# Kernel optimization log

Hardware: AMD Instinct MI355X
Metric: run time of the kernel (lower is better)

Reference implementation:

```python
import jax, jax.numpy as jnp
import numpy as np

B, N, F_IN, E, TOPK = 64, 1024, 64, 128, 32
NEG_SLOPE = 0.2  # GAT leaky-relu slope


def setup_inputs() -> dict:
    key = jax.random.key(0)
    ks = jax.random.split(key, 7)
    x = jax.random.normal(ks[0], (B, N, F_IN), dtype=jnp.float32)
    emb = jax.random.normal(ks[1], (N, E), dtype=jnp.float32)            # nn.Embedding table
    W_fe = jax.random.normal(ks[2], (F_IN, E), dtype=jnp.float32) / np.sqrt(F_IN).astype(np.float32)
    a_src = jax.random.normal(ks[3], (2 * E,), dtype=jnp.float32) * 0.05
    a_dst = jax.random.normal(ks[4], (2 * E,), dtype=jnp.float32) * 0.05
    lin_W = jax.random.normal(ks[5], (E, 1), dtype=jnp.float32) / np.sqrt(E).astype(np.float32)
    lin_b = jnp.zeros((1,), dtype=jnp.float32)
    return {"x": x, "emb": emb, "W_fe": W_fe, "a_src": a_src, "a_dst": a_dst,
            "lin_W": lin_W, "lin_b": lin_b}


def reference(x, emb, W_fe, a_src, a_dst, lin_W, lin_b):
    b, n, _ = x.shape
    e_dim = emb.shape[-1]
    # --- cosine-similarity topk graph construction (shared across batch) ---
    norm = jnp.linalg.norm(emb, axis=-1, keepdims=True)                  # [N,1]
    sim = (emb @ emb.T) / (norm @ norm.T)                                # [N,N]
    idx = jax.lax.top_k(sim, TOPK)[1]                                    # [N,K] int32 neighbor (target) nodes
    # --- graph attention feature extraction ---
    h = jnp.einsum('bnf,fe->bne', x, W_fe)                               # [B,N,E] projected node features
    g = jnp.concatenate([h, jnp.broadcast_to(emb, (b, n, e_dim))], -1)   # [B,N,2E] feat || embedding
    e_s = g @ a_src                                                      # [B,N] source attention term
    e_d = g @ a_dst                                                      # [B,N] target attention term
    # edges: source i repeated TOPK times -> targets idx[i]; softmax over each node's K neighbors
    scores = jax.nn.leaky_relu(e_s[:, :, None] + e_d[:, idx], NEG_SLOPE)  # [B,N,K]
    alpha = jax.nn.softmax(scores, axis=-1)                              # [B,N,K]
    h_dst = h[:, idx, :]                                                 # [B,N,K,E] gathered neighbor feats
    out = jnp.einsum('bnk,bnke->bne', alpha, h_dst)                      # aggregate messages
    out = jax.nn.relu(out)
    # --- linear readout ---
    y = out @ lin_W + lin_b                                              # [B,N,1]
    return y[..., 0]                                                     # [B,N]
```

## Files before the change

### kernel.cpp

```cpp
#include <hip/hip_runtime.h>
#include <math.h>

#define BB 64
#define NN 1024
#define F_IN 64
#define EE 128
#define TOPK 32
#define NEG_SLOPE 0.2f

typedef unsigned int uint;
typedef unsigned short ushort;
typedef unsigned long long ull;
typedef __attribute__((ext_vector_type(8))) short short8;
typedef __attribute__((ext_vector_type(4))) float f32x4;

static __device__ __forceinline__ uint f2bf(float f) {
  const uint x = __float_as_uint(f);
  return (x + 0x7fffu + ((x >> 16) & 1u)) >> 16;
}
static __device__ __forceinline__ float bf_lo(uint u) {
  return __uint_as_float(u << 16);
}
static __device__ __forceinline__ float bf_hi_raw(uint u) {
  return __uint_as_float(u);
}
static __device__ __forceinline__ uint fmono(float f) {
  uint u = __float_as_uint(f);
  return (u & 0x80000000u) ? ~u : (u | 0x80000000u);
}
static __device__ __forceinline__ ull umax64(ull a, ull b) {
  return a > b ? a : b;
}
static __device__ __forceinline__ ull umin64(ull a, ull b) {
  return a < b ? a : b;
}
static __device__ __forceinline__ ull shfl_xor64(ull v, int mask) {
  const uint lo = __shfl_xor((uint)v, mask);
  const uint hi = __shfl_xor((uint)(v >> 32), mask);
  return ((ull)hi << 32) | lo;
}

__global__ __launch_bounds__(256) void k2a_sim(
    const float* __restrict__ emb, const float* __restrict__ a_src,
    const float* __restrict__ a_dst, const float* __restrict__ W_fe,
    uint* __restrict__ keys, float* __restrict__ u_src,
    float* __restrict__ u_dst, ushort* __restrict__ wt) {
  __shared__ float ei[8][130];
  __shared__ float ej[64][130];
  const int t = threadIdx.x, wid = t >> 6, lane = t & 63;
  const int i0 = (blockIdx.x >> 2) * 8;
  const int jbase = (blockIdx.x & 3) * 256;

  if ((blockIdx.x & 3) == 0) {
    const int row = i0 + 2 * wid + (lane >> 5);
    const int ll = lane & 31;
    const float* er = emb + (size_t)row * EE;
    float us = 0.f, ud = 0.f;
#pragma unroll
    for (int c0 = 0; c0 < EE; c0 += 32) {
      const int c = c0 + ll;
      const float e = er[c];
      us += e * a_src[EE + c];
      ud += e * a_dst[EE + c];
    }
#pragma unroll
    for (int o = 1; o <= 16; o <<= 1) {
      us += __shfl_xor(us, o);
      ud += __shfl_xor(ud, o);
    }
    if (ll == 0) {
      u_src[row] = us;
      u_dst[row] = ud;
    }
  } else if ((blockIdx.x & 3) == 1 && (blockIdx.x >> 2) < 32) {
    const int g = (blockIdx.x >> 2) * 256 + t;
    const int n = g >> 6, k = g & 63;
    wt[g] = (ushort)f2bf(W_fe[k * EE + n]);
  }

  {
    const int r = t >> 5, c4 = t & 31;
    const float4 v = *(const float4*)&emb[(size_t)(i0 + r) * EE + c4 * 4];
    *(float2*)&ei[r][c4 * 4] = make_float2(v.x, v.y);
    *(float2*)&ei[r][c4 * 4 + 2] = make_float2(v.z, v.w);
  }

  const int ia = i0 + wid * 2;

  for (int ch = 0; ch < 4; ++ch) {
    const int j0 = jbase + ch * 64;
#pragma unroll
    for (int p = 0; p < 8; ++p) {
      const int g = p * 256 + t;
      const int r = g >> 5, c4 = g & 31;
      const float4 v = *(const float4*)&emb[(size_t)(j0 + r) * EE + c4 * 4];
      *(float2*)&ej[r][c4 * 4] = make_float2(v.x, v.y);
      *(float2*)&ej[r][c4 * 4 + 2] = make_float2(v.z, v.w);
    }
    __syncthreads();

    float a0 = 0.f, a1 = 0.f, sq = 0.f;
#pragma unroll 8
    for (int d2 = 0; d2 < 64; ++d2) {
      const float2 e = *(const float2*)&ej[lane][2 * d2];
      const float2 wa = *(const float2*)&ei[wid * 2][2 * d2];
      const float2 wb = *(const float2*)&ei[wid * 2 + 1][2 * d2];
      a0 += e.x * wa.x + e.y * wa.y;
      a1 += e.x * wb.x + e.y * wb.y;
      sq += e.x * e.x + e.y * e.y;
    }
    const int jg = j0 + lane;
    const float rj = rsqrtf(sq);
    keys[(size_t)ia * NN + jg] = fmono(a0 * rj);
    keys[(size_t)(ia + 1) * NN + jg] = fmono(a1 * rj);
    __syncthreads();
  }
}

__global__ __launch_bounds__(256) void k23(
    const uint* __restrict__ keys, int* __restrict__ idx_out,
    const float* __restrict__ x, const ushort* __restrict__ wt,
    const float* __restrict__ a_src, const float* __restrict__ a_dst,
    const float* __restrict__ u_src, const float* __restrict__ u_dst,
    uint* __restrict__ h2, float* __restrict__ es, float* __restrict__ ed) {
  __shared__ ull cand[128];
  const int t = threadIdx.x, wid = t >> 6, lane = t & 63;

  if (blockIdx.x < NN) {
    const int row = blockIdx.x;

    const int jb = wid * 256 + lane * 4;
    const uint4 kv = *(const uint4*)&keys[(size_t)row * NN + jb];
    ull xr[4];
    xr[0] = ((ull)kv.x << 32) | (uint)(jb + 0);
    xr[1] = ((ull)kv.y << 32) | (uint)(jb + 1);
    xr[2] = ((ull)kv.z << 32) | (uint)(jb + 2);
    xr[3] = ((ull)kv.w << 32) | (uint)(jb + 3);

#pragma unroll
    for (int k = 2; k <= 256; k <<= 1) {
#pragma unroll
      for (int d = 128; d >= 1; d >>= 1) {
        if (d > (k >> 1)) continue;
        if (d >= 4) {
          const int pl = d >> 2;
          const bool lower = (lane & pl) == 0;
#pragma unroll
          for (int r = 0; r < 4; ++r) {
            const ull o = shfl_xor64(xr[r], pl);
            const bool desc = (((lane * 4 + r) & k) == 0);
            const bool keepmax = (desc == lower);
            xr[r] = keepmax ? umax64(xr[r], o) : umin64(xr[r], o);
          }
        } else if (d == 2) {
#pragma unroll
          for (int r = 0; r < 2; ++r) {
            const bool desc = (((lane * 4 + r) & k) == 0);
            const ull hi = umax64(xr[r], xr[r + 2]);
            const ull lo = umin64(xr[r], xr[r + 2]);
            xr[r] = desc ? hi : lo;
            xr[r + 2] = desc ? lo : hi;
          }
        } else {
#pragma unroll
          for (int r = 0; r < 4; r += 2) {
            const bool desc = (((lane * 4 + r) & k) == 0);
            const ull hi = umax64(xr[r], xr[r + 1]);
            const ull lo = umin64(xr[r], xr[r + 1]);
            xr[r] = desc ? hi : lo;
            xr[r + 1] = desc ? lo : hi;
          }
        }
      }
    }
    if (lane < 8) {
#pragma unroll
      for (int r = 0; r < 4; ++r) cand[wid * 32 + lane * 4 + r] = xr[r];
    }
    __syncthreads();

    if (wid == 0) {
      ull k0 = cand[2 * lane];
      ull k1 = cand[2 * lane + 1];
#pragma unroll
      for (int k = 2; k <= 128; k <<= 1) {
#pragma unroll
        for (int d = k >> 1; d > 0; d >>= 1) {
          if (d >= 2) {
            const int pl = d >> 1;
            const ull o0 = shfl_xor64(k0, pl);
            const ull o1 = shfl_xor64(k1, pl);
            const bool keepmax =
                ((lane & (k >> 1)) == 0) == ((lane & pl) == 0);
            k0 = keepmax ? umax64(k0, o0) : umin64(k0, o0);
            k1 = keepmax ? umax64(k1, o1) : umin64(k1, o1);
          } else {
            const bool keepmax0 = ((lane & (k >> 1)) == 0);
            const ull hi = umax64(k0, k1), lo = umin64(k0, k1);
            k0 = keepmax0 ? hi : lo;
            k1 = keepmax0 ? lo : hi;
          }
        }
      }
      if (lane < 16) {
        int* ro = idx_out + (size_t)row * TOPK;
        ro[2 * lane] = (int)(k0 & 1023u);
        ro[2 * lane + 1] = (int)(k1 & 1023u);
      }
    }
  } else {
    const int row0 = (blockIdx.x - NN) * 64;
    const int nn = lane & 15, quad = lane >> 4;
    const int row0w = row0 + wid * 16;

    short8 af[2];
#pragma unroll
    for (int s = 0; s < 2; ++s) {
      const float* xr2 = x + (size_t)(row0w + nn) * F_IN + s * 32 + quad * 8;
      const float4 v0 = *(const float4*)&xr2[0];
      const float4 v1 = *(const float4*)&xr2[4];
      af[s][0] = (short)f2bf(v0.x);
      af[s][1] = (short)f2bf(v0.y);
      af[s][2] = (short)f2bf(v0.z);
      af[s][3] = (short)f2bf(v0.w);
      af[s][4] = (short)f2bf(v1.x);
      af[s][5] = (short)f2bf(v1.y);
      af[s][6] = (short)f2bf(v1.z);
      af[s][7] = (short)f2bf(v1.w);
    }

    f32x4 acc[8];
#pragma unroll
    for (int T = 0; T < 8; ++T) acc[T] = (f32x4){0.f, 0.f, 0.f, 0.f};

#pragma unroll
    for (int T = 0; T < 8; ++T) {
#pragma unroll
      for (int s = 0; s < 2; ++s) {
        const short8 bf =
            *(const short8*)&wt[(T * 16 + nn) * F_IN + s * 32 + quad * 8];
        acc[T] =
            __builtin_amdgcn_mfma_f32_16x16x32_bf16(af[s], bf, acc[T], 0, 0, 0);
      }
    }

    const int growbase = row0w + quad * 4;
#pragma unroll
    for (int reg = 0; reg < 4; ++reg) {
      uint* hr = h2 + (size_t)(growbase + reg) * 64 + nn;
#pragma unroll
      for (int T4 = 0; T4 < 4; ++T4) {
        hr[T4 * 16] =
            f2bf(acc[2 * T4][reg]) | (f2bf(acc[2 * T4 + 1][reg]) << 16);
      }
    }
    float ae[8], de[8];
#pragma unroll
    for (int T = 0; T < 8; ++T) {
      ae[T] = a_src[T * 16 + nn];
      de[T] = a_dst[T * 16 + nn];
    }
#pragma unroll
    for (int reg = 0; reg < 4; ++reg) {
      float ps = 0.f, pd = 0.f;
#pragma unroll
      for (int T = 0; T < 8; ++T) {
        ps += acc[T][reg] * ae[T];
        pd += acc[T][reg] * de[T];
      }
#pragma unroll
      for (int o = 1; o <= 8; o <<= 1) {
        ps += __shfl_xor(ps, o);
        pd += __shfl_xor(pd, o);
      }
      if (nn == 0) {
        const int grow = growbase + reg;
        const int node = grow & (NN - 1);
        es[grow] = ps + u_src[node];
        ed[grow] = pd + u_dst[node];
      }
    }
  }
}

__global__ __launch_bounds__(256) void k4_attn(
    const uint* __restrict__ h2, const float* __restrict__ es,
    const float* __restrict__ ed, const int* __restrict__ idx,
    const float* __restrict__ lin_W, const float* __restrict__ lin_b,
    float* __restrict__ y) {
  const int t = threadIdx.x, wid = t >> 6, lane = t & 63;
  const int blk = blockIdx.x;
  const int xcd = blk & 7, x = blk >> 3;
  const int b = xcd * 8 + (x >> 7);
  const int half = lane >> 5, ll = lane & 31;
  const int nh = (x & 127) * 8 + wid * 2 + half;
  const int sub2 = ll >> 4, c16 = ll & 15;
  const int pbase = half * 128 + sub2 * 4;

  const float* edb = ed + (size_t)b * NN;
  const float* esb = es + (size_t)b * NN;
  const char* hb = (const char*)(h2 + (size_t)b * NN * 64);

  const int j = idx[nh * TOPK + ll];
  const int off = j << 8;
  int offk[16];
#pragma unroll
  for (int k = 0; k < 16; ++k)
    offk[k] = __builtin_amdgcn_ds_bpermute(pbase + k * 8, off);
  uint4 tv[16];
#pragma unroll
  for (int k = 0; k < 16; ++k)
    tv[k] = *(const uint4*)(hb + ((uint)offk[k] + c16 * 16));

  const float esv = esb[nh];
  float s = esv + edb[j];
  s = s > 0.f ? s : NEG_SLOPE * s;
  const float p = __expf(s);
  float dsum = p;
#pragma unroll
  for (int o = 1; o <= 16; o <<= 1) dsum += __shfl_xor(dsum, o);
  const float w = p * (1.0f / dsum);
  float wk[16];
#pragma unroll
  for (int k = 0; k < 16; ++k)
    wk[k] = __uint_as_float(
        __builtin_amdgcn_ds_bpermute(pbase + k * 8, __float_as_uint(w)));

  float lwlo[4], lwhi[4];
#pragma unroll
  for (int i = 0; i < 4; ++i) {
    const int c = 4 * c16 + i;
    const int t4 = c >> 4, nn2 = c & 15;
    lwlo[i] = lin_W[t4 * 32 + nn2];
    lwhi[i] = lin_W[t4 * 32 + 16 + nn2];
  }
  const float bias = lin_b[0];

  float acc[8];
#pragma unroll
  for (int i = 0; i < 8; i++) acc[i] = 0.f;
#pragma unroll
  for (int k = 0; k < 16; ++k) {
    const float ak = wk[k];
    const uint4 u = tv[k];
    acc[0] += ak * bf_lo(u.x);
    acc[1] += ak * bf_hi_raw(u.x);
    acc[2] += ak * bf_lo(u.y);
    acc[3] += ak * bf_hi_raw(u.y);
    acc[4] += ak * bf_lo(u.z);
    acc[5] += ak * bf_hi_raw(u.z);
    acc[6] += ak * bf_lo(u.w);
    acc[7] += ak * bf_hi_raw(u.w);
  }
#pragma unroll
  for (int i = 0; i < 8; i++) {
    acc[i] += __shfl_xor(acc[i], 16);
    acc[i] = acc[i] > 0.f ? acc[i] : 0.f;
  }
  float r = acc[0] * lwlo[0] + acc[1] * lwhi[0] + acc[2] * lwlo[1] +
            acc[3] * lwhi[1] + acc[4] * lwlo[2] + acc[5] * lwhi[2] +
            acc[6] * lwlo[3] + acc[7] * lwhi[3];
#pragma unroll
  for (int o = 8; o > 0; o >>= 1) r += __shfl_xor(r, o);
  if (ll == 0) y[(size_t)b * NN + nh] = r + bias;
}

extern "C" void kernel_launch(void* const* d_in, const int* in_sizes, int n_in,
                              void* d_out, int out_size, void* d_ws,
                              size_t ws_size, hipStream_t stream) {
  const float* x = (const float*)d_in[0];
  const float* emb = (const float*)d_in[1];
  const float* W_fe = (const float*)d_in[2];
  const float* a_src = (const float*)d_in[3];
  const float* a_dst = (const float*)d_in[4];
  const float* lin_W = (const float*)d_in[5];
  const float* lin_b = (const float*)d_in[6];
  float* y = (float*)d_out;

  char* ws = (char*)d_ws;
  float* u_src = (float*)(ws + 4096);
  float* u_dst = (float*)(ws + 8192);
  int* idx = (int*)(ws + 16384);
  float* es = (float*)(ws + 147456);
  float* ed = (float*)(ws + 409600);
  uint* h2 = (uint*)(ws + 671744);
  uint* keys = (uint*)(ws + 17448960);
  ushort* wt = (ushort*)(ws + 21643264);

  k2a_sim<<<512, 256, 0, stream>>>(emb, a_src, a_dst, W_fe, keys, u_src,
                                   u_dst, wt);
  k23<<<2048, 256, 0, stream>>>(keys, idx, x, wt, a_src, a_dst, u_src, u_dst,
                                h2, es, ed);
  k4_attn<<<8192, 256, 0, stream>>>(h2, es, ed, idx, lin_W, lin_b, y);
}
```

Before: 135.1 us.

## Widen sim LDS loads, shorten top-k merge, give each attention wave more neighbors

The similarity kernel pads its LDS rows to 132 floats with 16-byte alignment so it can use float4 stores and loads, halving LDS instruction count. The final top-k merge of 128 candidates is replaced by two parallel 64-element bitonic merges followed by a single 64-lane merge, rather than a full 128-element bitonic sort. The attention kernel now has each 16-lane group handle all 32 neighbors of one node, issuing two gather batches per lane instead of splitting the neighbors across 32 lanes. This removes the cross-half shuffle, halves the grid, and keeps more loads in flight per thread, at the cost of higher register pressure.

Result: no change. 132.9 us (-1.6%).

```diff
diff --git a/kernel.cpp b/kernel.cpp
--- a/kernel.cpp
+++ b/kernel.cpp
@@ -45,8 +45,8 @@
     const float* __restrict__ a_dst, const float* __restrict__ W_fe,
     uint* __restrict__ keys, float* __restrict__ u_src,
     float* __restrict__ u_dst, ushort* __restrict__ wt) {
-  __shared__ float ei[8][130];
-  __shared__ float ej[64][130];
+  __shared__ __align__(16) float ei[8][132];
+  __shared__ __align__(16) float ej[64][132];
   const int t = threadIdx.x, wid = t >> 6, lane = t & 63;
   const int i0 = (blockIdx.x >> 2) * 8;
   const int jbase = (blockIdx.x & 3) * 256;
@@ -81,8 +81,7 @@
   {
     const int r = t >> 5, c4 = t & 31;
     const float4 v = *(const float4*)&emb[(size_t)(i0 + r) * EE + c4 * 4];
-    *(float2*)&ei[r][c4 * 4] = make_float2(v.x, v.y);
-    *(float2*)&ei[r][c4 * 4 + 2] = make_float2(v.z, v.w);
+    *(float4*)&ei[r][c4 * 4] = v;
   }
 
   const int ia = i0 + wid * 2;
@@ -94,20 +93,19 @@
       const int g = p * 256 + t;
       const int r = g >> 5, c4 = g & 31;
       const float4 v = *(const float4*)&emb[(size_t)(j0 + r) * EE + c4 * 4];
-      *(float2*)&ej[r][c4 * 4] = make_float2(v.x, v.y);
-      *(float2*)&ej[r][c4 * 4 + 2] = make_float2(v.z, v.w);
+      *(float4*)&ej[r][c4 * 4] = v;
     }
     __syncthreads();
 
     float a0 = 0.f, a1 = 0.f, sq = 0.f;
 #pragma unroll 8
-    for (int d2 = 0; d2 < 64; ++d2) {
-      const float2 e = *(const float2*)&ej[lane][2 * d2];
-      const float2 wa = *(const float2*)&ei[wid * 2][2 * d2];
-      const float2 wb = *(const float2*)&ei[wid * 2 + 1][2 * d2];
-      a0 += e.x * wa.x + e.y * wa.y;
-      a1 += e.x * wb.x + e.y * wb.y;
-      sq += e.x * e.x + e.y * e.y;
+    for (int d4 = 0; d4 < 32; ++d4) {
+      const float4 e = *(const float4*)&ej[lane][4 * d4];
+      const float4 wa = *(const float4*)&ei[wid * 2][4 * d4];
+      const float4 wb = *(const float4*)&ei[wid * 2 + 1][4 * d4];
+      a0 += e.x * wa.x + e.y * wa.y + e.z * wa.z + e.w * wa.w;
+      a1 += e.x * wb.x + e.y * wb.y + e.z * wb.z + e.w * wb.w;
+      sq += e.x * e.x + e.y * e.y + e.z * e.z + e.w * e.w;
     }
     const int jg = j0 + lane;
     const float rj = rsqrtf(sq);
@@ -179,34 +177,26 @@
     }
     __syncthreads();
 
+    if (wid < 2) {
+      const int base = wid * 64;
+      ull v = (lane < 32) ? cand[base + lane] : cand[base + 95 - lane];
+#pragma unroll
+      for (int d = 32; d >= 1; d >>= 1) {
+        const ull o = shfl_xor64(v, d);
+        v = ((lane & d) == 0) ? umax64(v, o) : umin64(v, o);
+      }
+      if (lane < 32) cand[base + lane] = v;
+    }
+    __syncthreads();
+
     if (wid == 0) {
-      ull k0 = cand[2 * lane];
-      ull k1 = cand[2 * lane + 1];
-#pragma unroll
-      for (int k = 2; k <= 128; k <<= 1) {
-#pragma unroll
-        for (int d = k >> 1; d > 0; d >>= 1) {
-          if (d >= 2) {
-            const int pl = d >> 1;
-            const ull o0 = shfl_xor64(k0, pl);
-            const ull o1 = shfl_xor64(k1, pl);
-            const bool keepmax =
-                ((lane & (k >> 1)) == 0) == ((lane & pl) == 0);
-            k0 = keepmax ? umax64(k0, o0) : umin64(k0, o0);
-            k1 = keepmax ? umax64(k1, o1) : umin64(k1, o1);
-          } else {
-            const bool keepmax0 = ((lane & (k >> 1)) == 0);
-            const ull hi = umax64(k0, k1), lo = umin64(k0, k1);
-            k0 = keepmax0 ? hi : lo;
-            k1 = keepmax0 ? lo : hi;
-          }
-        }
-      }
-      if (lane < 16) {
-        int* ro = idx_out + (size_t)row * TOPK;
-        ro[2 * lane] = (int)(k0 & 1023u);
-        ro[2 * lane + 1] = (int)(k1 & 1023u);
-      }
+      ull v = (lane < 32) ? cand[lane] : cand[127 - lane];
+#pragma unroll
+      for (int d = 32; d >= 1; d >>= 1) {
+        const ull o = shfl_xor64(v, d);
+        v = ((lane & d) == 0) ? umax64(v, o) : umin64(v, o);
+      }
+      if (lane < 32) idx_out[(size_t)row * TOPK + lane] = (int)(v & 1023u);
     }
   } else {
     const int row0 = (blockIdx.x - NN) * 64;
@@ -291,45 +281,58 @@
   const int t = threadIdx.x, wid = t >> 6, lane = t & 63;
   const int blk = blockIdx.x;
   const int xcd = blk & 7, x = blk >> 3;
-  const int b = xcd * 8 + (x >> 7);
-  const int half = lane >> 5, ll = lane & 31;
-  const int nh = (x & 127) * 8 + wid * 2 + half;
-  const int sub2 = ll >> 4, c16 = ll & 15;
-  const int pbase = half * 128 + sub2 * 4;
+  const int b = xcd * 8 + (x >> 6);
+  const int q = lane >> 4, ll = lane & 15;
+  const int n = (x & 63) * 16 + wid * 4 + q;
+  const int pbase = q * 64;
 
   const float* edb = ed + (size_t)b * NN;
   const float* esb = es + (size_t)b * NN;
   const char* hb = (const char*)(h2 + (size_t)b * NN * 64);
 
-  const int j = idx[nh * TOPK + ll];
-  const int off = j << 8;
-  int offk[16];
+  const int j0 = idx[n * TOPK + ll];
+  const int j1 = idx[n * TOPK + 16 + ll];
+  const int off0 = j0 << 8, off1 = j1 << 8;
+  int offA[16], offB[16];
+#pragma unroll
+  for (int k = 0; k < 16; ++k) {
+    offA[k] = __builtin_amdgcn_ds_bpermute(pbase + k * 4, off0);
+    offB[k] = __builtin_amdgcn_ds_bpermute(pbase + k * 4, off1);
+  }
+  uint4 tvA[16];
 #pragma unroll
   for (int k = 0; k < 16; ++k)
-    offk[k] = __builtin_amdgcn_ds_bpermute(pbase + k * 8, off);
-  uint4 tv[16];
+    tvA[k] = *(const uint4*)(hb + ((uint)offA[k] + ll * 16));
+  uint4 tvB[16];
 #pragma unroll
   for (int k = 0; k < 16; ++k)
-    tv[k] = *(const uint4*)(hb + ((uint)offk[k] + c16 * 16));
-
-  const float esv = esb[nh];
-  float s = esv + edb[j];
-  s = s > 0.f ? s : NEG_SLOPE * s;
-  const float p = __expf(s);
-  float dsum = p;
-#pragma unroll
-  for (int o = 1; o <= 16; o <<= 1) dsum += __shfl_xor(dsum, o);
-  const float w = p * (1.0f / dsum);
-  float wk[16];
-#pragma unroll
-  for (int k = 0; k < 16; ++k)
-    wk[k] = __uint_as_float(
-        __builtin_amdgcn_ds_bpermute(pbase + k * 8, __float_as_uint(w)));
+    tvB[k] = *(const uint4*)(hb + ((uint)offB[k] + ll * 16));
+
+  const float esv = esb[n];
+  float s0 = esv + edb[j0];
+  float s1 = esv + edb[j1];
+  s0 = s0 > 0.f ? s0 : NEG_SLOPE * s0;
+  s1 = s1 > 0.f ? s1 : NEG_SLOPE * s1;
+  const float p0 = __expf(s0);
+  const float p1 = __expf(s1);
+  float dsum = p0 + p1;
+#pragma unroll
+  for (int o = 1; o <= 8; o <<= 1) dsum += __shfl_xor(dsum, o);
+  const float rs = 1.0f / dsum;
+  const float w0 = p0 * rs, w1 = p1 * rs;
+  float wkA[16], wkB[16];
+#pragma unroll
+  for (int k = 0; k < 16; ++k) {
+    wkA[k] = __uint_as_float(
+        __builtin_amdgcn_ds_bpermute(pbase + k * 4, __float_as_uint(w0)));
+    wkB[k] = __uint_as_float(
+        __builtin_amdgcn_ds_bpermute(pbase + k * 4, __float_as_uint(w1)));
+  }
 
   float lwlo[4], lwhi[4];
 #pragma unroll
   for (int i = 0; i < 4; ++i) {
-    const int c = 4 * c16 + i;
+    const int c = 4 * ll + i;
     const int t4 = c >> 4, nn2 = c & 15;
     lwlo[i] = lin_W[t4 * 32 + nn2];
     lwhi[i] = lin_W[t4 * 32 + 16 + nn2];
@@ -341,8 +344,8 @@
   for (int i = 0; i < 8; i++) acc[i] = 0.f;
 #pragma unroll
   for (int k = 0; k < 16; ++k) {
-    const float ak = wk[k];
-    const uint4 u = tv[k];
+    const float ak = wkA[k];
+    const uint4 u = tvA[k];
     acc[0] += ak * bf_lo(u.x);
     acc[1] += ak * bf_hi_raw(u.x);
     acc[2] += ak * bf_lo(u.y);
@@ -353,16 +356,28 @@
     acc[7] += ak * bf_hi_raw(u.w);
   }
 #pragma unroll
-  for (int i = 0; i < 8; i++) {
-    acc[i] += __shfl_xor(acc[i], 16);
-    acc[i] = acc[i] > 0.f ? acc[i] : 0.f;
-  }
-  float r = acc[0] * lwlo[0] + acc[1] * lwhi[0] + acc[2] * lwlo[1] +
-            acc[3] * lwhi[1] + acc[4] * lwlo[2] + acc[5] * lwhi[2] +
-            acc[6] * lwlo[3] + acc[7] * lwhi[3];
-#pragma unroll
-  for (int o = 8; o > 0; o >>= 1) r += __shfl_xor(r, o);
-  if (ll == 0) y[(size_t)b * NN + nh] = r + bias;
+  for (int k = 0; k < 16; ++k) {
+    const float ak = wkB[k];
+    const uint4 u = tvB[k];
+    acc[0] += ak * bf_lo(u.x);
+    acc[1] += ak * bf_hi_raw(u.x);
+    acc[2] += ak * bf_lo(u.y);
+    acc[3] += ak * bf_hi_raw(u.y);
+    acc[4] += ak * bf_lo(u.z);
+    acc[5] += ak * bf_hi_raw(u.z);
+    acc[6] += ak * bf_lo(u.w);
+    acc[7] += ak * bf_hi_raw(u.w);
+  }
+  float r = 0.f;
+#pragma unroll
+  for (int i = 0; i < 4; ++i) {
+    const float a0 = acc[2 * i] > 0.f ? acc[2 * i] : 0.f;
+    const float a1 = acc[2 * i + 1] > 0.f ? acc[2 * i + 1] : 0.f;
+    r += a0 * lwlo[i] + a1 * lwhi[i];
+  }
+#pragma unroll
+  for (int o = 1; o <= 8; o <<= 1) r += __shfl_xor(r, o);
+  if (ll == 0) y[(size_t)b * NN + n] = r + bias;
 }
 
 extern "C" void kernel_launch(void* const* d_in, const int* in_sizes, int n_in,
@@ -391,5 +406,5 @@
                                    u_dst, wt);
   k23<<<2048, 256, 0, stream>>>(keys, idx, x, wt, a_src, a_dst, u_src, u_dst,
                                 h2, es, ed);
-  k4_attn<<<8192, 256, 0, stream>>>(h2, es, ed, idx, lin_W, lin_b, y);
-}
+  k4_attn<<<4096, 256, 0, stream>>>(h2, es, ed, idx, lin_W, lin_b, y);
+}
```
